# Performance work log

Hardware: AMD Instinct MI355X
Metric: run time of the kernel (lower is better)

## Reference

```python
import jax, jax.numpy as jnp
import numpy as np

B, D, NUM_HOP, NUM_REL = 8192, 512, 8, 2000  # batch, input_dim, num_hop, num_relation
TAU = 1.0


def setup_inputs() -> dict:
    key = jax.random.key(0)
    ks = jax.random.split(key, 7)
    s = 1.0 / np.sqrt(D)  # PyTorch GRU uniform init bound
    return {
        "query": jax.random.normal(ks[0], (B, D), jnp.float32),
        "W_ih": jax.random.uniform(ks[1], (3 * D, D), jnp.float32, -s, s),
        "W_hh": jax.random.uniform(ks[2], (3 * D, D), jnp.float32, -s, s),
        "b_ih": jax.random.uniform(ks[3], (3 * D,), jnp.float32, -s, s),
        "b_hh": jax.random.uniform(ks[4], (3 * D,), jnp.float32, -s, s),
        "relation": jax.random.normal(ks[5], (2 * NUM_REL, D), jnp.float32),
        "eos": jax.random.normal(ks[6], (1, D), jnp.float32),
    }


def gru_cell(x, h, W_ih, W_hh, b_ih, b_hh):
    # PyTorch nn.GRU cell, gate order (r, z, n)
    gi = x @ W_ih.T + b_ih  # [B, 3D]
    gh = h @ W_hh.T + b_hh  # [B, 3D]
    ir, iz, i_n = jnp.split(gi, 3, axis=-1)
    hr, hz, h_n = jnp.split(gh, 3, axis=-1)
    r = jax.nn.sigmoid(ir + hr)
    z = jax.nn.sigmoid(iz + hz)
    n = jnp.tanh(i_n + r * h_n)
    return (1.0 - z) * n + z * h


def reference(query, W_ih, W_hh, b_ih, b_hh, relation, eos):
    # gru over seq [query, eos] starting from h0 = 0; hidden[1:] == final hx for 1 layer
    h0 = jnp.zeros_like(query)
    h1 = gru_cell(query, h0, W_ih, W_hh, b_ih, b_hh)
    hidden = gru_cell(jnp.broadcast_to(eos, query.shape), h1, W_ih, W_hh, b_ih, b_hh)

    def step(h, _):
        score = jnp.einsum('bd,rd->br', h, relation)          # [B, 2R]
        attention = jax.nn.softmax(score / TAU, axis=-1)
        subgoal = jnp.einsum('br,rd->bd', attention, relation)  # [B, D]
        h_new = gru_cell(subgoal, h, W_ih, W_hh, b_ih, b_hh)
        return h_new, subgoal

    _, subgoals = jax.lax.scan(step, hidden, None, length=NUM_HOP)  # [NUM_HOP, B, D]
    subgoals = jnp.moveaxis(subgoals, 0, 1)  # [B, NUM_HOP, D]
    masks = jnp.ones(subgoals.shape[:-1], dtype=bool)
    return subgoals, masks
```

## Files before the change

### kernel.cpp

```cpp
#include <hip/hip_runtime.h>


typedef _Float16 f16;
typedef _Float16 f16x8 __attribute__((ext_vector_type(8)));
typedef _Float16 f16x4 __attribute__((ext_vector_type(4)));
typedef float    f32x4 __attribute__((ext_vector_type(4)));

constexpr int BATCH = 8192;
constexpr int DDIM  = 512;
constexpr int D3    = 1536;
constexpr int NRELT = 4000;
constexpr int NRELP = 4096;
constexpr int NHOP  = 8;

#define MFMA16(a,b,c) __builtin_amdgcn_mfma_f32_16x16x32_f16((a),(b),(c),0,0,0)
#define BAR()   __builtin_amdgcn_s_barrier()
#define FENCE() asm volatile("" ::: "memory")
#define SCHED0() __builtin_amdgcn_sched_barrier(0)

__device__ __forceinline__ void gll16(const void* g, void* l) {
  __builtin_amdgcn_global_load_lds(
      (const __attribute__((address_space(1))) unsigned int*)g,
      (__attribute__((address_space(3))) unsigned int*)l, 16, 0, 0);
}

__global__ __launch_bounds__(256) void k_split(const float* __restrict__ src,
                                               f16* __restrict__ hi, f16* __restrict__ lo, int n) {
  int i = blockIdx.x * 256 + threadIdx.x;
  if (i >= n) return;
  float v = src[i];
  f16 h = (f16)v;
  hi[i] = h;
  lo[i] = (f16)(v - (float)h);
}

__global__ __launch_bounds__(256) void k_prep_rel(const float* __restrict__ rel,
    f16* __restrict__ rhi, f16* __restrict__ rlo,
    f16* __restrict__ thi, f16* __restrict__ tlo) {
  int i = blockIdx.x * 256 + threadIdx.x;
  if (i >= NRELP * DDIM) return;
  int r = i >> 9, d = i & 511;
  float v = (r < NRELT) ? rel[i] : 0.f;
  f16 h = (f16)v, l = (f16)(v - (float)h);
  rhi[i] = h; rlo[i] = l;
  thi[(size_t)d * NRELP + r] = h;
  tlo[(size_t)d * NRELP + r] = l;
}

__global__ __launch_bounds__(64) void k_gieos(const float* __restrict__ W,
                                              const float* __restrict__ eos,
                                              float* __restrict__ out) {
  int o = blockIdx.x;
  float s = 0.f;
  for (int i = threadIdx.x; i < DDIM; i += 64) s += W[(size_t)o * DDIM + i] * eos[i];
  for (int off = 32; off; off >>= 1) s += __shfl_xor(s, off);
  if (threadIdx.x == 0) out[o] = s;
}

template<int EPI>
__device__ __forceinline__ void gemm_core(
    const f16* __restrict__ Ahi, const f16* __restrict__ Alo, int lda,
    const f16* __restrict__ Bhi, const f16* __restrict__ Blo, int ldb,
    float* __restrict__ Cout, f16* __restrict__ Chi, f16* __restrict__ Clo,
    int ldc, int m0, int n0, int kst, int nt, f16* lds)
{
  const int tid  = threadIdx.x;
  const int lane = tid & 63;
  const int wave = tid >> 6;
  const int wm = wave >> 2;
  const int wn = wave & 3;
  const int rb = lane & 15;
  const int sl = lane >> 4;
  const int srow = lane >> 2;

  auto stage2 = [&](int buf, int p, int k0) {
    const f16* src = (p == 0) ? Ahi : (p == 1) ? Alo : (p == 2) ? Bhi : Blo;
    const int ld   = (p < 2) ? lda : ldb;
    const int base = (p < 2) ? m0 : n0;
    f16* pl = lds + ((buf * 4 + p) << 13);
    #pragma unroll
    for (int c = 0; c < 2; ++c) {
      const int r0 = wave * 16 + c * 128;
      const int lr = r0 + srow;
      const int slot = (lane & 3) ^ ((lr >> 1) & 3);
      gll16(src + (size_t)(base + lr) * ld + k0 + slot * 8, pl + r0 * 32);
    }
  };
  auto rd = [&](int buf, int p, int lr) -> f16x8 {
    const int off = lr * 64 + ((sl ^ ((lr >> 1) & 3)) << 4);
    return *(const f16x8*)((const char*)(lds + ((buf * 4 + p) << 13)) + off);
  };

  stage2(0, 0, kst); stage2(0, 1, kst); stage2(0, 2, kst); stage2(0, 3, kst);

  f32x4 acc[8][4] = {};
  f16x8 ah[4], al[4], bh0[2], bl0[2], bh1[2], bl1[2];

  for (int t = 0; t < nt; ++t) {
    const int cur = t & 1;
    const bool more = (t + 1 < nt);
    const int kn = kst + (t + 1) * 32;

    asm volatile("s_waitcnt vmcnt(0)" ::: "memory");
    BAR(); FENCE();
    if (more) stage2(cur ^ 1, 0, kn);
    #pragma unroll
    for (int f = 0; f < 4; ++f) {
      ah[f] = rd(cur, 0, wm * 128 + f * 16 + rb);
      al[f] = rd(cur, 1, wm * 128 + f * 16 + rb);
    }
    #pragma unroll
    for (int n = 0; n < 2; ++n) {
      bh0[n] = rd(cur, 2, wn * 64 + n * 16 + rb);
      bl0[n] = rd(cur, 3, wn * 64 + n * 16 + rb);
    }
    FENCE(); BAR(); FENCE();
    __builtin_amdgcn_s_setprio(1);
    #pragma unroll
    for (int f = 0; f < 4; ++f)
      #pragma unroll
      for (int n = 0; n < 2; ++n) {
        acc[f][n] = MFMA16(ah[f], bh0[n], acc[f][n]);
        acc[f][n] = MFMA16(ah[f], bl0[n], acc[f][n]);
        acc[f][n] = MFMA16(al[f], bh0[n], acc[f][n]);
      }
    __builtin_amdgcn_s_setprio(0);
    SCHED0();

    if (more) stage2(cur ^ 1, 1, kn);
    #pragma unroll
    for (int n = 0; n < 2; ++n) {
      bh1[n] = rd(cur, 2, wn * 64 + 32 + n * 16 + rb);
      bl1[n] = rd(cur, 3, wn * 64 + 32 + n * 16 + rb);
    }
    FENCE(); BAR(); FENCE();
    __builtin_amdgcn_s_setprio(1);
    #pragma unroll
    for (int f = 0; f < 4; ++f)
      #pragma unroll
      for (int n = 0; n < 2; ++n) {
        acc[f][2 + n] = MFMA16(ah[f], bh1[n], acc[f][2 + n]);
        acc[f][2 + n] = MFMA16(ah[f], bl1[n], acc[f][2 + n]);
        acc[f][2 + n] = MFMA16(al[f], bh1[n], acc[f][2 + n]);
      }
    __builtin_amdgcn_s_setprio(0);
    SCHED0();

    if (more) stage2(cur ^ 1, 2, kn);
    #pragma unroll
    for (int f = 0; f < 4; ++f) {
      ah[f] = rd(cur, 0, wm * 128 + 64 + f * 16 + rb);
      al[f] = rd(cur, 1, wm * 128 + 64 + f * 16 + rb);
    }
    FENCE(); BAR(); FENCE();
    __builtin_amdgcn_s_setprio(1);
    #pragma unroll
    for (int f = 0; f < 4; ++f)
      #pragma unroll
      for (int n = 0; n < 2; ++n) {
        acc[4 + f][2 + n] = MFMA16(ah[f], bh1[n], acc[4 + f][2 + n]);
        acc[4 + f][2 + n] = MFMA16(ah[f], bl1[n], acc[4 + f][2 + n]);
        acc[4 + f][2 + n] = MFMA16(al[f], bh1[n], acc[4 + f][2 + n]);
      }
    __builtin_amdgcn_s_setprio(0);
    SCHED0();

    if (more) stage2(cur ^ 1, 3, kn);
    FENCE(); BAR(); FENCE();
    __builtin_amdgcn_s_setprio(1);
    #pragma unroll
    for (int f = 0; f < 4; ++f)
      #pragma unroll
      for (int n = 0; n < 2; ++n) {
        acc[4 + f][n] = MFMA16(ah[f], bh0[n], acc[4 + f][n]);
        acc[4 + f][n] = MFMA16(ah[f], bl0[n], acc[4 + f][n]);
        acc[4 + f][n] = MFMA16(al[f], bh0[n], acc[4 + f][n]);
      }
    __builtin_amdgcn_s_setprio(0);
    SCHED0();
  }

  #pragma unroll
  for (int fm = 0; fm < 8; ++fm)
    #pragma unroll
    for (int fn = 0; fn < 4; ++fn)
      #pragma unroll
      for (int r = 0; r < 4; ++r) {
        const int gr = m0 + wm * 128 + fm * 16 + sl * 4 + r;
        const int gc = n0 + wn * 64 + fn * 16 + rb;
        const float v = acc[fm][fn][r];
        if constexpr (EPI == 0) {
          Cout[(size_t)gr * ldc + gc] = v;
        } else {
          const f16 vh = (f16)v;
          Chi[(size_t)gr * ldc + gc] = vh;
          Clo[(size_t)gr * ldc + gc] = (f16)(v - (float)vh);
        }
      }
}

template<int EPI>
__global__ __launch_bounds__(512, 2)
void k_gemm8(const f16* __restrict__ Ahi, const f16* __restrict__ Alo, int lda,
             const f16* __restrict__ Bhi, const f16* __restrict__ Blo, int ldb,
             float* __restrict__ Cout, f16* __restrict__ Chi, f16* __restrict__ Clo,
             int ldc, int K, int gy, int nblocks)
{
  __shared__ __align__(16) f16 lds[2 * 4 * 256 * 32];
  const int bid = blockIdx.x;
  const int id2 = (bid & 7) * (nblocks >> 3) + (bid >> 3);
  const int m = id2 & 31;
  const int rest = id2 >> 5;
  const int n = rest % gy;
  const int z = rest / gy;
  float* Co = Cout ? Cout + (size_t)z * BATCH * (size_t)ldc : nullptr;
  gemm_core<EPI>(Ahi, Alo, lda, Bhi, Blo, ldb, Co, Chi, Clo, ldc,
                 m * 256, n * 256, z * K, K / 32, lds);
}

__global__ __launch_bounds__(512, 2)
void k_gemm8_gru(const f16* __restrict__ xhi, const f16* __restrict__ xlo,
                 const f16* __restrict__ hhi, const f16* __restrict__ hlo,
                 const f16* __restrict__ wihhi, const f16* __restrict__ wihlo,
                 const f16* __restrict__ whhhi, const f16* __restrict__ whhlo,
                 float* __restrict__ gi, float* __restrict__ gh)
{
  __shared__ __align__(16) f16 lds[2 * 4 * 256 * 32];
  const int bid = blockIdx.x;
  const int id2 = (bid & 7) * 48 + (bid >> 3);
  const int m = id2 & 31;
  const int nn = id2 >> 5;
  const bool second = nn >= 6;
  gemm_core<0>(second ? hhi : xhi, second ? hlo : xlo, DDIM,
               second ? whhhi : wihhi, second ? whhlo : wihlo, DDIM,
               second ? gh : gi, nullptr, nullptr, D3,
               m * 256, (second ? nn - 6 : nn) * 256, 0, DDIM / 32, lds);
}

__global__ __launch_bounds__(256)
void k_softmax(f16* __restrict__ Shi, f16* __restrict__ Slo) {
  const int row = blockIdx.x;
  f16* phi = Shi + (size_t)row * NRELP;
  f16* plo = Slo + (size_t)row * NRELP;
  const int tid = threadIdx.x, lane = tid & 63, wv = tid >> 6;
  const int ng = (tid < 232) ? 4 : 3;
  f32x4 v[4];
  float mx = -3.402823e38f;
  #pragma unroll
  for (int i = 0; i < 4; ++i)
    if (i < ng) {
      f16x4 hv = *(const f16x4*)(phi + (tid + 256 * i) * 4);
      f16x4 lv = *(const f16x4*)(plo + (tid + 256 * i) * 4);
      #pragma unroll
      for (int j = 0; j < 4; ++j) v[i][j] = (float)hv[j] + (float)lv[j];
      mx = fmaxf(fmaxf(fmaxf(mx, v[i][0]), fmaxf(v[i][1], v[i][2])), v[i][3]);
    }
  float l = 0.f;
  #pragma unroll
  for (int i = 0; i < 4; ++i)
    if (i < ng)
      l += __expf(v[i][0] - mx) + __expf(v[i][1] - mx)
         + __expf(v[i][2] - mx) + __expf(v[i][3] - mx);
  #pragma unroll
  for (int off = 1; off < 64; off <<= 1) {
    float om = __shfl_xor(mx, off), ol = __shfl_xor(l, off);
    float nm = fmaxf(mx, om);
    l = l * __expf(mx - nm) + ol * __expf(om - nm);
    mx = nm;
  }
  __shared__ float sm[4], slr[4];
  if (lane == 0) { sm[wv] = mx; slr[wv] = l; }
  __syncthreads();
  const float fm = fmaxf(fmaxf(sm[0], sm[1]), fmaxf(sm[2], sm[3]));
  const float fl = slr[0] * __expf(sm[0] - fm) + slr[1] * __expf(sm[1] - fm)
                 + slr[2] * __expf(sm[2] - fm) + slr[3] * __expf(sm[3] - fm);
  const float il = 1.f / fl;
  #pragma unroll
  for (int i = 0; i < 4; ++i)
    if (i < ng) {
      f16x4 oh, ol;
      #pragma unroll
      for (int j = 0; j < 4; ++j) {
        const float pv = __expf(v[i][j] - fm) * il;
        const f16 ph = (f16)pv;
        oh[j] = ph;
        ol[j] = (f16)(pv - (float)ph);
      }
      *(f16x4*)(phi + (tid + 256 * i) * 4) = oh;
      *(f16x4*)(plo + (tid + 256 * i) * 4) = ol;
    }
  if (tid < 24) {
    f16x4 z = {(f16)0.f, (f16)0.f, (f16)0.f, (f16)0.f};
    *(f16x4*)(phi + (1000 + tid) * 4) = z;
    *(f16x4*)(plo + (1000 + tid) * 4) = z;
  }
}

__global__ __launch_bounds__(256)
void k_subred(const float* __restrict__ Cp, float* __restrict__ outp,
              f16* __restrict__ xhi, f16* __restrict__ xlo, int hop) {
  const int idx = blockIdx.x * 256 + threadIdx.x;
  const int b = idx >> 7, d4 = (idx & 127) * 4;
  const size_t o = (size_t)b * DDIM + d4;
  f32x4 s = *(const f32x4*)(Cp + o);
  s += *(const f32x4*)(Cp + (size_t)BATCH * DDIM + o);
  s += *(const f32x4*)(Cp + 2 * (size_t)BATCH * DDIM + o);
  s += *(const f32x4*)(Cp + 3 * (size_t)BATCH * DDIM + o);
  *(f32x4*)(outp + (size_t)b * (NHOP * DDIM) + (size_t)hop * DDIM + d4) = s;
  f16x4 vh, vl;
  #pragma unroll
  for (int j = 0; j < 4; ++j) {
    const f16 ph = (f16)s[j];
    vh[j] = ph;
    vl[j] = (f16)(s[j] - (float)ph);
  }
  *(f16x4*)(xhi + o) = vh;
  *(f16x4*)(xlo + o) = vl;
}

__global__ __launch_bounds__(256)
void k_gates(const float* __restrict__ gi, const float* __restrict__ givec,
             const float* __restrict__ gh,
             const float* __restrict__ bih, const float* __restrict__ bhh,
             const float* __restrict__ hin, float* __restrict__ hout,
             f16* __restrict__ hhi, f16* __restrict__ hlo)
{
  const int idx = blockIdx.x * 256 + threadIdx.x;
  const int b  = idx >> 7;
  const int d4 = (idx & 127) * 4;
  f32x4 ir, iz, inn;
  if (gi) {
    const float* g = gi + (size_t)b * D3 + d4;
    ir  = *(const f32x4*)(g);
    iz  = *(const f32x4*)(g + DDIM);
    inn = *(const f32x4*)(g + 2 * DDIM);
  } else {
    ir  = *(const f32x4*)(givec + d4);
    iz  = *(const f32x4*)(givec + DDIM + d4);
    inn = *(const f32x4*)(givec + 2 * DDIM + d4);
  }
  ir  += *(const f32x4*)(bih + d4);
  iz  += *(const f32x4*)(bih + DDIM + d4);
  inn += *(const f32x4*)(bih + 2 * DDIM + d4);
  f32x4 hr = {0.f, 0.f, 0.f, 0.f}, hz = {0.f, 0.f, 0.f, 0.f}, hn = {0.f, 0.f, 0.f, 0.f};
  if (gh) {
    const float* g = gh + (size_t)b * D3 + d4;
    hr = *(const f32x4*)(g);
    hz = *(const f32x4*)(g + DDIM);
    hn = *(const f32x4*)(g + 2 * DDIM);
  }
  hr += *(const f32x4*)(bhh + d4);
  hz += *(const f32x4*)(bhh + DDIM + d4);
  hn += *(const f32x4*)(bhh + 2 * DDIM + d4);
  f32x4 hp = {0.f, 0.f, 0.f, 0.f};
  if (hin) hp = *(const f32x4*)(hin + (size_t)b * DDIM + d4);
  f32x4 hv; f16x4 vh, vl;
  #pragma unroll
  for (int j = 0; j < 4; ++j) {
    const float r = 1.f / (1.f + __expf(-(ir[j] + hr[j])));
    const float z = 1.f / (1.f + __expf(-(iz[j] + hz[j])));
    const float n = tanhf(inn[j] + r * hn[j]);
    const float h = (1.f - z) * n + z * hp[j];
    hv[j] = h;
    const f16 ph = (f16)h;
    vh[j] = ph;
    vl[j] = (f16)(h - (float)ph);
  }
  *(f32x4*)(hout + (size_t)b * DDIM + d4) = hv;
  *(f16x4*)(hhi + (size_t)b * DDIM + d4) = vh;
  *(f16x4*)(hlo + (size_t)b * DDIM + d4) = vl;
}

__global__ __launch_bounds__(256) void k_ones(float* __restrict__ o, int n) {
  int i = blockIdx.x * 256 + threadIdx.x;
  if (i < n) o[i] = 1.0f;
}

extern "C" void kernel_launch(void* const* d_in, const int* in_sizes, int n_in,
                              void* d_out, int out_size, void* d_ws, size_t ws_size,
                              hipStream_t stream)
{
  const float* query = (const float*)d_in[0];
  const float* W_ih  = (const float*)d_in[1];
  const float* W_hh  = (const float*)d_in[2];
  const float* b_ih  = (const float*)d_in[3];
  const float* b_hh  = (const float*)d_in[4];
  const float* rel   = (const float*)d_in[5];
  const float* eos   = (const float*)d_in[6];
  float* out = (float*)d_out;
  (void)in_sizes; (void)n_in; (void)out_size; (void)ws_size;

  char* w = (char*)d_ws;
  f16* SPhi    = (f16*)w;   w += (size_t)BATCH * NRELP * 2;
  f16* SPlo    = (f16*)w;   w += (size_t)BATCH * NRELP * 2;
  float* Cpart = (float*)w; w += (size_t)4 * BATCH * DDIM * 4;
  float* hbuf  = (float*)w; w += (size_t)BATCH * DDIM * 4;
  f16* h_hi    = (f16*)w;   w += (size_t)BATCH * DDIM * 2;
  f16* h_lo    = (f16*)w;   w += (size_t)BATCH * DDIM * 2;
  f16* x_hi    = (f16*)w;   w += (size_t)BATCH * DDIM * 2;
  f16* x_lo    = (f16*)w;   w += (size_t)BATCH * DDIM * 2;
  f16* wih_hi  = (f16*)w;   w += (size_t)D3 * DDIM * 2;
  f16* wih_lo  = (f16*)w;   w += (size_t)D3 * DDIM * 2;
  f16* whh_hi  = (f16*)w;   w += (size_t)D3 * DDIM * 2;
  f16* whh_lo  = (f16*)w;   w += (size_t)D3 * DDIM * 2;
  f16* rel_hi  = (f16*)w;   w += (size_t)NRELP * DDIM * 2;
  f16* rel_lo  = (f16*)w;   w += (size_t)NRELP * DDIM * 2;
  f16* relT_hi = (f16*)w;   w += (size_t)DDIM * NRELP * 2;
  f16* relT_lo = (f16*)w;   w += (size_t)DDIM * NRELP * 2;
  float* gieos = (float*)w; w += (size_t)D3 * 4;
  float* gi = (float*)SPhi;
  float* gh = (float*)SPhi + (size_t)BATCH * D3;

  k_split<<<(BATCH * DDIM + 255) / 256, 256, 0, stream>>>(query, x_hi, x_lo, BATCH * DDIM);
  k_split<<<(D3 * DDIM + 255) / 256, 256, 0, stream>>>(W_ih, wih_hi, wih_lo, D3 * DDIM);
  k_split<<<(D3 * DDIM + 255) / 256, 256, 0, stream>>>(W_hh, whh_hi, whh_lo, D3 * DDIM);
  k_prep_rel<<<(NRELP * DDIM + 255) / 256, 256, 0, stream>>>(rel, rel_hi, rel_lo, relT_hi, relT_lo);
  k_gieos<<<D3, 64, 0, stream>>>(W_ih, eos, gieos);

  const int ggrid = BATCH * DDIM / 4 / 256;

  k_gemm8<0><<<192, 512, 0, stream>>>(x_hi, x_lo, DDIM, wih_hi, wih_lo, DDIM,
      gi, nullptr, nullptr, D3, DDIM, 6, 192);
  k_gates<<<ggrid, 256, 0, stream>>>(gi, nullptr, nullptr, b_ih, b_hh, nullptr, hbuf, h_hi, h_lo);

  k_gemm8<0><<<192, 512, 0, stream>>>(h_hi, h_lo, DDIM, whh_hi, whh_lo, DDIM,
      gh, nullptr, nullptr, D3, DDIM, 6, 192);
  k_gates<<<ggrid, 256, 0, stream>>>(nullptr, gieos, gh, b_ih, b_hh, hbuf, hbuf, h_hi, h_lo);

  for (int hop = 0; hop < NHOP; ++hop) {
    k_gemm8<1><<<512, 512, 0, stream>>>(h_hi, h_lo, DDIM, rel_hi, rel_lo, DDIM,
        nullptr, SPhi, SPlo, NRELP, DDIM, 16, 512);
    k_softmax<<<BATCH, 256, 0, stream>>>(SPhi, SPlo);
    k_gemm8<0><<<256, 512, 0, stream>>>(SPhi, SPlo, NRELP,
        relT_hi, relT_lo, NRELP, Cpart, nullptr, nullptr, DDIM, 1024, 2, 256);
    k_subred<<<ggrid, 256, 0, stream>>>(Cpart, out, x_hi, x_lo, hop);
    k_gemm8_gru<<<384, 512, 0, stream>>>(x_hi, x_lo, h_hi, h_lo,
        wih_hi, wih_lo, whh_hi, whh_lo, gi, gh);
    k_gates<<<ggrid, 256, 0, stream>>>(gi, nullptr, gh, b_ih, b_hh, hbuf, hbuf, h_hi, h_lo);
  }

  k_ones<<<(BATCH * NHOP + 255) / 256, 256, 0, stream>>>(out + (size_t)BATCH * NHOP * DDIM, BATCH * NHOP);
}
```

Before: 3.331 ms.

## Restructure split-fp16 GEMM main loop into per-plane stages with partial vmcnt waits

Reorganizes the 3-pass hi/lo fp16 GEMM inner loop into six 4x4 MFMA quads, each consuming one hi or lo operand plane, and reorders the global-to-LDS staging so that each plane is waited on with a partial vmcnt instead of a full vmcnt(0) at the top of the iteration. The aim is to overlap next-tile loads with MFMA work more finely and to cut register pressure by reading fewer fragments at a time. In exchange it adds barriers per iteration, and the correctness of the LDS buffer reuse depends on the exact ordering of the vmcnt counts.

```diff
diff --git a/kernel.cpp b/kernel.cpp
--- a/kernel.cpp
+++ b/kernel.cpp
@@ -17,6 +17,7 @@
 #define BAR()   __builtin_amdgcn_s_barrier()
 #define FENCE() asm volatile("" ::: "memory")
 #define SCHED0() __builtin_amdgcn_sched_barrier(0)
+#define VM(n) asm volatile("s_waitcnt vmcnt(" #n ")" ::: "memory")
 
 __device__ __forceinline__ void gll16(const void* g, void* l) {
   __builtin_amdgcn_global_load_lds(
@@ -56,6 +57,17 @@
   for (int off = 32; off; off >>= 1) s += __shfl_xor(s, off);
   if (threadIdx.x == 0) out[o] = s;
 }
+
+#define MQUAD(AOP, BOP, FMOFF) \
+  __builtin_amdgcn_s_setprio(1); \
+  _Pragma("unroll") \
+  for (int fm = 0; fm < 4; ++fm) { \
+    _Pragma("unroll") \
+    for (int fn = 0; fn < 4; ++fn) \
+      acc[(FMOFF) + fm][fn] = MFMA16(AOP[fm], BOP[fn], acc[(FMOFF) + fm][fn]); \
+  } \
+  __builtin_amdgcn_s_setprio(0); \
+  SCHED0();
 
 template<int EPI>
 __device__ __forceinline__ void gemm_core(
@@ -91,93 +103,56 @@
     return *(const f16x8*)((const char*)(lds + ((buf * 4 + p) << 13)) + off);
   };
 
-  stage2(0, 0, kst); stage2(0, 1, kst); stage2(0, 2, kst); stage2(0, 3, kst);
+  stage2(0, 2, kst); stage2(0, 0, kst); stage2(0, 1, kst); stage2(0, 3, kst);
 
   f32x4 acc[8][4] = {};
-  f16x8 ah[4], al[4], bh0[2], bl0[2], bh1[2], bl1[2];
+  f16x8 ah[4], al[4], bh[4], bl[4];
+  const int A0 = wm * 128, B0 = wn * 64;
 
   for (int t = 0; t < nt; ++t) {
     const int cur = t & 1;
+    const int nxt = cur ^ 1;
     const bool more = (t + 1 < nt);
     const int kn = kst + (t + 1) * 32;
 
-    asm volatile("s_waitcnt vmcnt(0)" ::: "memory");
-    BAR(); FENCE();
-    if (more) stage2(cur ^ 1, 0, kn);
-    #pragma unroll
-    for (int f = 0; f < 4; ++f) {
-      ah[f] = rd(cur, 0, wm * 128 + f * 16 + rb);
-      al[f] = rd(cur, 1, wm * 128 + f * 16 + rb);
-    }
-    #pragma unroll
-    for (int n = 0; n < 2; ++n) {
-      bh0[n] = rd(cur, 2, wn * 64 + n * 16 + rb);
-      bl0[n] = rd(cur, 3, wn * 64 + n * 16 + rb);
-    }
-    FENCE(); BAR(); FENCE();
-    __builtin_amdgcn_s_setprio(1);
-    #pragma unroll
-    for (int f = 0; f < 4; ++f)
-      #pragma unroll
-      for (int n = 0; n < 2; ++n) {
-        acc[f][n] = MFMA16(ah[f], bh0[n], acc[f][n]);
-        acc[f][n] = MFMA16(ah[f], bl0[n], acc[f][n]);
-        acc[f][n] = MFMA16(al[f], bh0[n], acc[f][n]);
-      }
-    __builtin_amdgcn_s_setprio(0);
-    SCHED0();
-
-    if (more) stage2(cur ^ 1, 1, kn);
-    #pragma unroll
-    for (int n = 0; n < 2; ++n) {
-      bh1[n] = rd(cur, 2, wn * 64 + 32 + n * 16 + rb);
-      bl1[n] = rd(cur, 3, wn * 64 + 32 + n * 16 + rb);
-    }
-    FENCE(); BAR(); FENCE();
-    __builtin_amdgcn_s_setprio(1);
-    #pragma unroll
-    for (int f = 0; f < 4; ++f)
-      #pragma unroll
-      for (int n = 0; n < 2; ++n) {
-        acc[f][2 + n] = MFMA16(ah[f], bh1[n], acc[f][2 + n]);
-        acc[f][2 + n] = MFMA16(ah[f], bl1[n], acc[f][2 + n]);
-        acc[f][2 + n] = MFMA16(al[f], bh1[n], acc[f][2 + n]);
-      }
-    __builtin_amdgcn_s_setprio(0);
-    SCHED0();
-
-    if (more) stage2(cur ^ 1, 2, kn);
-    #pragma unroll
-    for (int f = 0; f < 4; ++f) {
-      ah[f] = rd(cur, 0, wm * 128 + 64 + f * 16 + rb);
-      al[f] = rd(cur, 1, wm * 128 + 64 + f * 16 + rb);
-    }
-    FENCE(); BAR(); FENCE();
-    __builtin_amdgcn_s_setprio(1);
-    #pragma unroll
-    for (int f = 0; f < 4; ++f)
-      #pragma unroll
-      for (int n = 0; n < 2; ++n) {
-        acc[4 + f][2 + n] = MFMA16(ah[f], bh1[n], acc[4 + f][2 + n]);
-        acc[4 + f][2 + n] = MFMA16(ah[f], bl1[n], acc[4 + f][2 + n]);
-        acc[4 + f][2 + n] = MFMA16(al[f], bh1[n], acc[4 + f][2 + n]);
-      }
-    __builtin_amdgcn_s_setprio(0);
-    SCHED0();
-
-    if (more) stage2(cur ^ 1, 3, kn);
-    FENCE(); BAR(); FENCE();
-    __builtin_amdgcn_s_setprio(1);
-    #pragma unroll
-    for (int f = 0; f < 4; ++f)
-      #pragma unroll
-      for (int n = 0; n < 2; ++n) {
-        acc[4 + f][n] = MFMA16(ah[f], bh0[n], acc[4 + f][n]);
-        acc[4 + f][n] = MFMA16(ah[f], bl0[n], acc[4 + f][n]);
-        acc[4 + f][n] = MFMA16(al[f], bh0[n], acc[4 + f][n]);
-      }
-    __builtin_amdgcn_s_setprio(0);
-    SCHED0();
+    if (more) { stage2(nxt, 2, kn); VM(6); } else { VM(4); }
+    FENCE(); BAR(); FENCE();
+    #pragma unroll
+    for (int f = 0; f < 4; ++f) ah[f] = rd(cur, 0, A0 + f * 16 + rb);
+    #pragma unroll
+    for (int f = 0; f < 4; ++f) bh[f] = rd(cur, 2, B0 + f * 16 + rb);
+    FENCE(); BAR(); FENCE();
+    MQUAD(ah, bh, 0)
+
+    if (more) { stage2(nxt, 0, kn); VM(6); } else { VM(2); }
+    FENCE(); BAR(); FENCE();
+    #pragma unroll
+    for (int f = 0; f < 4; ++f) al[f] = rd(cur, 1, A0 + f * 16 + rb);
+    FENCE(); BAR(); FENCE();
+    MQUAD(al, bh, 0)
+
+    if (more) { stage2(nxt, 1, kn); VM(6); } else { VM(0); }
+    FENCE(); BAR(); FENCE();
+    #pragma unroll
+    for (int f = 0; f < 4; ++f) bl[f] = rd(cur, 3, B0 + f * 16 + rb);
+    FENCE(); BAR(); FENCE();
+    MQUAD(ah, bl, 0)
+
+    if (more) stage2(nxt, 3, kn);
+    FENCE(); BAR(); FENCE();
+    #pragma unroll
+    for (int f = 0; f < 4; ++f) ah[f] = rd(cur, 0, A0 + 64 + f * 16 + rb);
+    FENCE(); BAR(); FENCE();
+    MQUAD(ah, bl, 4)
+
+    FENCE(); BAR(); FENCE();
+    MQUAD(ah, bh, 4)
+
+    FENCE(); BAR(); FENCE();
+    #pragma unroll
+    for (int f = 0; f < 4; ++f) al[f] = rd(cur, 1, A0 + 64 + f * 16 + rb);
+    FENCE(); BAR(); FENCE();
+    MQUAD(al, bh, 4)
   }
 
   #pragma unroll
```

New measurement: 3.129 ms. 6.1% less time.
